# Kernel tuning notes

Measured on AMD Instinct MI355X. Metric: run time of the kernel, lower is better.

The kernel has to match this reference:

```python
import jax, jax.numpy as jnp
import numpy as np
import math

DIM = 512
HEADS = 16
HD = DIM // HEADS
HT, WT = 32, 32          # trained input_resolution
LT = HT * WT             # trained_len
TBL = (2 * HT - 1) * (2 * WT - 1)  # 3969 rows in relative_coords_table
CPB_HID = 512


def _l2norm(a, eps=1e-12):
    n = jnp.linalg.norm(a, axis=-1, keepdims=True)
    return a / jnp.maximum(n, eps)


def setup_inputs() -> dict:
    key = jax.random.key(0)
    ks = jax.random.split(key, 10)
    B, N = 8, 1024
    std = 0.02
    return {
        "x": jax.random.normal(ks[0], (B, N, DIM), jnp.float32),
        "qkv_w": jax.random.normal(ks[1], (3 * DIM, DIM), jnp.float32) * std,
        "qkv_b": jnp.zeros((3 * DIM,), jnp.float32),
        "proj_w": jax.random.normal(ks[2], (DIM, DIM), jnp.float32) * std,
        "proj_b": jnp.zeros((DIM,), jnp.float32),
        # softplus-inverse init: softplus(temperature) == 1/0.24
        "temperature": jnp.log(jnp.exp(jnp.ones((HEADS, 1, 1), jnp.float32) / 0.24) - 1.0),
        "query_embedding": jax.random.normal(ks[3], (HEADS, 1, HD), jnp.float32) * 0.02,
        "cpb_fc1_w": jax.random.normal(ks[4], (CPB_HID, 2), jnp.float32) * std,
        "cpb_fc1_b": jnp.zeros((CPB_HID,), jnp.float32),
        "cpb_fc2_w": jax.random.normal(ks[5], (HEADS, CPB_HID), jnp.float32) * std,
        "cpb_fc2_b": jnp.zeros((HEADS,), jnp.float32),
        "relative_coords_table": jax.random.uniform(ks[6], (TBL, 2), jnp.float32, -1.0, 1.0),
        "relative_pos_index": jax.random.randint(ks[7], (LT * LT,), 0, TBL, jnp.int32),
        "seq_length_scale": jnp.float32(math.log(float(N))),
        "padding_mask": jnp.zeros((B, N), bool),
        "H": 32,
        "W": 32,
    }


def reference(x, qkv_w, qkv_b, proj_w, proj_b, temperature, query_embedding,
              cpb_fc1_w, cpb_fc1_b, cpb_fc2_w, cpb_fc2_b,
              relative_coords_table, seq_length_scale,
              relative_pos_index, padding_mask, H, W):
    B, N, C = x.shape
    # qkv projection -> [B, N, 3, heads, hd] -> per-tensor [B, heads, N, hd]
    qkv = (x @ qkv_w.T + qkv_b).reshape(B, N, 3, HEADS, HD)
    q, k, v = (jnp.transpose(qkv[:, :, i], (0, 2, 1, 3)) for i in range(3))

    # continuous position bias MLP: [TBL, 2] -> [TBL, heads]
    t = jnp.maximum(relative_coords_table @ cpb_fc1_w.T + cpb_fc1_b, 0.0)
    t = t @ cpb_fc2_w.T + cpb_fc2_b                       # [TBL, heads]
    rb = t.T[:, relative_pos_index]                       # [heads, LT*LT]
    rb = rb.reshape(HEADS, LT, HT, WT)
    rb = jax.image.resize(rb, (HEADS, LT, H, W), 'bilinear')   # interp key axis
    rb = rb.reshape(HEADS, LT, N).transpose(0, 2, 1).reshape(HEADS, N, HT, WT)
    rb = jax.image.resize(rb, (HEADS, N, H, W), 'bilinear')    # interp query axis
    rb = rb.reshape(HEADS, N, N).transpose(0, 2, 1)             # [heads, N, N]

    scale = jax.nn.softplus(temperature) * seq_length_scale     # [heads, 1, 1]
    qn = (_l2norm(q) + query_embedding[None]) * scale[None]     # [B, heads, N, hd]
    kn = _l2norm(k)
    attn = jnp.einsum('bhnd,bhmd->bhnm', qn, kn) + rb[None]     # [B, heads, N, N]
    attn = jax.nn.softmax(attn, axis=-1)
    out = jnp.einsum('bhnm,bhmd->bhnd', attn, v)
    out = out.transpose(0, 2, 1, 3).reshape(B, N, C)
    return out @ proj_w.T + proj_b
```

## Files before the change

### kernel.cpp

```cpp
#include <hip/hip_runtime.h>
#include <math.h>

#define BATCH 8
#define NSEQ  1024
#define DIMC  512
#define HEADS 16
#define HD    32
#define TBLN  3969
#define QROWS (BATCH*HEADS*NSEQ)

typedef __attribute__((ext_vector_type(8))) short bf16x8;
typedef __attribute__((ext_vector_type(4))) float f32x4;

__device__ __forceinline__ unsigned short f2bf(float f) {
  union { float f; unsigned u; } c; c.f = f;
  unsigned x = c.u + 0x7fffu + ((c.u >> 16) & 1u);
  return (unsigned short)(x >> 16);
}
__device__ __forceinline__ float bf2f(unsigned short h) {
  union { unsigned u; float f; } c; c.u = ((unsigned)h) << 16; return c.f;
}

__global__ __launch_bounds__(256) void split_kernel(
    const float* __restrict__ src, unsigned short* __restrict__ hi,
    unsigned short* __restrict__ lo, int n4)
{
  int gid = blockIdx.x * 256 + threadIdx.x;
  if (gid >= n4) return;
  float4 v = ((const float4*)src)[gid];
  float vv[4] = {v.x, v.y, v.z, v.w};
  unsigned short h[4], l[4];
#pragma unroll
  for (int i = 0; i < 4; ++i) {
    h[i] = f2bf(vv[i]);
    l[i] = f2bf(vv[i] - bf2f(h[i]));
  }
  uint2 hp, lp;
  hp.x = h[0] | ((unsigned)h[1] << 16); hp.y = h[2] | ((unsigned)h[3] << 16);
  lp.x = l[0] | ((unsigned)l[1] << 16); lp.y = l[2] | ((unsigned)l[3] << 16);
  ((uint2*)hi)[gid] = hp;
  ((uint2*)lo)[gid] = lp;
}

template<int EPI>
__global__ __launch_bounds__(256) void gemm_split_kernel(
    const unsigned short* __restrict__ Ah, const unsigned short* __restrict__ Al,
    const unsigned short* __restrict__ Wh, const unsigned short* __restrict__ Wl,
    const float* __restrict__ bias,
    float* __restrict__ o0p, float* __restrict__ o1p, float* __restrict__ o2p)
{
  const int K = DIMC;
  __shared__ __align__(16) unsigned short lds[4 * 4096];
  unsigned short* ldsAh = lds;
  unsigned short* ldsAl = lds + 4096;
  unsigned short* ldsBh = lds + 8192;
  unsigned short* ldsBl = lds + 12288;
  const int tid = threadIdx.x;
  const int wave = tid >> 6, lane = tid & 63;
  const int l16 = lane & 15, hi4 = lane >> 4;
  const int rowBase = blockIdx.y * 128, colBase = blockIdx.x * 128;
  const int warpRow = (wave >> 1) * 64, warpCol = (wave & 1) * 64;

  const int o0 = wave * 2048 + lane * 16;
  const int o1 = o0 + 1024;
  const int row0 = o0 >> 6, s0 = (o0 >> 4) & 3;
  const int row1 = o1 >> 6, s1 = (o1 >> 4) & 3;
  const int g0 = row0 * K + ((s0 ^ ((row0 >> 1) & 3)) << 3);
  const int g1 = row1 * K + ((s1 ^ ((row1 >> 1) & 3)) << 3);

  const unsigned short* A0h = Ah + (size_t)rowBase * K;
  const unsigned short* A0l = Al + (size_t)rowBase * K;
  const unsigned short* W0h = Wh + (size_t)colBase * K;
  const unsigned short* W0l = Wl + (size_t)colBase * K;

  f32x4 acc[4][4] = {};

  float biasv[4];
#pragma unroll
  for (int fj = 0; fj < 4; ++fj)
    biasv[fj] = bias[colBase + warpCol + fj * 16 + l16];

  int ra[4], rbq[4];
#pragma unroll
  for (int f = 0; f < 4; ++f) {
    int rowA = warpRow + f * 16 + l16;
    ra[f] = rowA * 64 + ((hi4 ^ ((rowA >> 1) & 3)) << 4);
    int rowB = warpCol + f * 16 + l16;
    rbq[f] = rowB * 64 + ((hi4 ^ ((rowB >> 1) & 3)) << 4);
  }

#define GLD(gsrc, ldst) __builtin_amdgcn_global_load_lds( \
      (const __attribute__((address_space(1))) unsigned int*)(gsrc), \
      (__attribute__((address_space(3))) unsigned int*)(ldst), 16, 0, 0)

  for (int k0 = 0; k0 < K; k0 += 32) {
    __syncthreads();
    GLD(A0h + k0 + g0, (char*)ldsAh + o0);
    GLD(A0h + k0 + g1, (char*)ldsAh + o1);
    GLD(A0l + k0 + g0, (char*)ldsAl + o0);
    GLD(A0l + k0 + g1, (char*)ldsAl + o1);
    GLD(W0h + k0 + g0, (char*)ldsBh + o0);
    GLD(W0h + k0 + g1, (char*)ldsBh + o1);
    GLD(W0l + k0 + g0, (char*)ldsBl + o0);
    GLD(W0l + k0 + g1, (char*)ldsBl + o1);
    __syncthreads();

    bf16x8 a_h[4], a_l[4], b_h[4], b_l[4];
#pragma unroll
    for (int f = 0; f < 4; ++f) {
      a_h[f] = *(const bf16x8*)((const char*)ldsAh + ra[f]);
      a_l[f] = *(const bf16x8*)((const char*)ldsAl + ra[f]);
      b_h[f] = *(const bf16x8*)((const char*)ldsBh + rbq[f]);
      b_l[f] = *(const bf16x8*)((const char*)ldsBl + rbq[f]);
    }
#pragma unroll
    for (int fi = 0; fi < 4; ++fi)
#pragma unroll
      for (int fj = 0; fj < 4; ++fj) {
        acc[fi][fj] = __builtin_amdgcn_mfma_f32_16x16x32_bf16(a_l[fi], b_h[fj], acc[fi][fj], 0, 0, 0);
        acc[fi][fj] = __builtin_amdgcn_mfma_f32_16x16x32_bf16(a_h[fi], b_l[fj], acc[fi][fj], 0, 0, 0);
        acc[fi][fj] = __builtin_amdgcn_mfma_f32_16x16x32_bf16(a_h[fi], b_h[fj], acc[fi][fj], 0, 0, 0);
      }
  }
#undef GLD

#pragma unroll
  for (int fi = 0; fi < 4; ++fi)
#pragma unroll
    for (int fj = 0; fj < 4; ++fj)
#pragma unroll
      for (int r = 0; r < 4; ++r) {
        int m = rowBase + warpRow + fi * 16 + hi4 * 4 + r;
        int c = colBase + warpCol + fj * 16 + l16;
        float val = acc[fi][fj][r] + biasv[fj];
        if (EPI == 0) {
          int b = m >> 10, n = m & 1023;
          int which = c >> 9, rem = c & 511;
          int hh = rem >> 5, d = rem & 31;
          float* dst = (which == 0) ? o0p : (which == 1) ? o1p : o2p;
          dst[(((size_t)b * HEADS + hh) * NSEQ + n) * HD + d] = val;
        } else {
          o0p[(size_t)m * DIMC + c] = val;
        }
      }
}

__global__ __launch_bounds__(256) void cpb_kernel(
    const float* __restrict__ table, const float* __restrict__ fc1w,
    const float* __restrict__ fc1b, const float* __restrict__ fc2w,
    const float* __restrict__ fc2b, float* __restrict__ tT)
{
  const int row = blockIdx.x;
  const float c0 = table[row*2], c1 = table[row*2+1];
  __shared__ float hid[512];
  __shared__ float red[256];
  const int tid = threadIdx.x;
  for (int j = tid; j < 512; j += 256)
    hid[j] = fmaxf(fmaf(c0, fc1w[j*2], fmaf(c1, fc1w[j*2+1], fc1b[j])), 0.f);
  __syncthreads();
  const int h = tid & 15, part = tid >> 4;
  float s = 0.f;
#pragma unroll
  for (int jj = 0; jj < 32; ++jj) {
    int j = part*32 + jj;
    s = fmaf(hid[j], fc2w[h*512 + j], s);
  }
  red[tid] = s;
  __syncthreads();
  if (tid < 16) {
    float t = fc2b[tid];
#pragma unroll
    for (int p = 0; p < 16; ++p) t += red[tid + p*16];
    tT[(size_t)tid * TBLN + row] = t;
  }
}

__global__ __launch_bounds__(256) void rb_gather_kernel(
    const float* __restrict__ tT, const int* __restrict__ rpi,
    unsigned short* __restrict__ rb)
{
  int gid = blockIdx.x * 256 + threadIdx.x;
  int idx = rpi[gid];
#pragma unroll
  for (int h = 0; h < 16; ++h)
    rb[(size_t)h * NSEQ * NSEQ + gid] = f2bf(tT[h * TBLN + idx]);
}

__global__ __launch_bounds__(256) void normsplit_kernel(
    const float* __restrict__ qb, const float* __restrict__ kb,
    const float* __restrict__ temperature, const float* __restrict__ qe,
    const float* __restrict__ sls,
    unsigned short* __restrict__ qh, unsigned short* __restrict__ ql,
    unsigned short* __restrict__ kh, unsigned short* __restrict__ kl)
{
  const int gid = blockIdx.x * 256 + threadIdx.x;
  const int lane = gid & 31;
  const int row = gid >> 5;
  const bool isQ = row < QROWS;
  const float* src = isQ ? qb : kb;
  const int r = isQ ? row : row - QROWS;
  float x = src[(size_t)r * HD + lane];
  float ss = x * x;
#pragma unroll
  for (int m = 16; m >= 1; m >>= 1) ss += __shfl_xor(ss, m);
  float y = x / fmaxf(sqrtf(ss), 1e-12f);
  if (isQ) {
    const int h = (r >> 10) & (HEADS - 1);
    float scale = log1pf(__expf(temperature[h])) * sls[0];
    y = (y + qe[h * HD + lane]) * scale;
  }
  unsigned short hi = f2bf(y);
  unsigned short lo = f2bf(y - bf2f(hi));
  size_t idx = (size_t)r * HD + lane;
  if (isQ) { qh[idx] = hi; ql[idx] = lo; }
  else     { kh[idx] = hi; kl[idx] = lo; }
}

__global__ __launch_bounds__(256) void vt_kernel(
    const float* __restrict__ vb, unsigned short* __restrict__ vt)
{
  __shared__ float tile[32][257];
  const int bh = blockIdx.x, ch = blockIdx.y;
  const int t = threadIdx.x;
  const float* src = vb + ((size_t)bh * NSEQ + ch * 256) * HD;
#pragma unroll
  for (int i = 0; i < 32; ++i) {
    int idx = i * 256 + t;
    tile[idx & 31][idx >> 5] = src[idx];
  }
  __syncthreads();
  unsigned short* dst = vt + (size_t)bh * HD * NSEQ + ch * 256;
#pragma unroll
  for (int i = 0; i < 32; ++i) {
    int idx = i * 256 + t;
    int d = idx >> 8, nl = idx & 255;
    dst[(size_t)d * NSEQ + nl] = f2bf(tile[d][nl]);
  }
}

__global__ __launch_bounds__(256, 4) void attn_mfma_kernel(
    const unsigned short* __restrict__ qh, const unsigned short* __restrict__ ql,
    const unsigned short* __restrict__ kh, const unsigned short* __restrict__ kl,
    const unsigned short* __restrict__ vt, const unsigned short* __restrict__ rb,
    unsigned short* __restrict__ aoh, unsigned short* __restrict__ aol)
{
  const int bh = blockIdx.x;
  const int h = bh & (HEADS - 1), b = bh >> 4;
  const int wave = threadIdx.x >> 6;
  const int lane = threadIdx.x & 63;
  const int l16 = lane & 15, hi4 = lane >> 4;
  const int qbase = blockIdx.y * 128 + wave * 32;

  bf16x8 qhf[2], qlf[2];
#pragma unroll
  for (int g = 0; g < 2; ++g) {
    size_t ro = ((size_t)bh * NSEQ + qbase + g * 16 + l16) * HD + hi4 * 8;
    qhf[g] = *(const bf16x8*)(qh + ro);
    qlf[g] = *(const bf16x8*)(ql + ro);
  }

  f32x4 accV[2][2] = {};
  float mst[2] = {-INFINITY, -INFINITY};
  float lst[2] = {0.f, 0.f};

  const int krow_p = 8 * (l16 >> 2) + (l16 & 3);

  for (int kt = 0; kt < NSEQ / 32; ++kt) {
    const int k0 = kt * 32;
    size_t kr0 = ((size_t)bh * NSEQ + k0 + krow_p) * HD + hi4 * 8;
    size_t kr1 = kr0 + 4 * HD;
    bf16x8 kh0 = *(const bf16x8*)(kh + kr0);
    bf16x8 kh1 = *(const bf16x8*)(kh + kr1);
    bf16x8 kl0 = *(const bf16x8*)(kl + kr0);
    bf16x8 kl1 = *(const bf16x8*)(kl + kr1);
    bf16x8 vt0 = *(const bf16x8*)(vt + ((size_t)bh * HD +  0 + l16) * NSEQ + k0 + hi4 * 8);
    bf16x8 vt1 = *(const bf16x8*)(vt + ((size_t)bh * HD + 16 + l16) * NSEQ + k0 + hi4 * 8);

#pragma unroll
    for (int g = 0; g < 2; ++g) {
      f32x4 D0 = {0.f, 0.f, 0.f, 0.f};
      f32x4 D1 = {0.f, 0.f, 0.f, 0.f};
      D0 = __builtin_amdgcn_mfma_f32_16x16x32_bf16(kh0, qhf[g], D0, 0, 0, 0);
      D0 = __builtin_amdgcn_mfma_f32_16x16x32_bf16(kh0, qlf[g], D0, 0, 0, 0);
      D0 = __builtin_amdgcn_mfma_f32_16x16x32_bf16(kl0, qhf[g], D0, 0, 0, 0);
      D1 = __builtin_amdgcn_mfma_f32_16x16x32_bf16(kh1, qhf[g], D1, 0, 0, 0);
      D1 = __builtin_amdgcn_mfma_f32_16x16x32_bf16(kh1, qlf[g], D1, 0, 0, 0);
      D1 = __builtin_amdgcn_mfma_f32_16x16x32_bf16(kl1, qhf[g], D1, 0, 0, 0);

      bf16x8 b8 = *(const bf16x8*)(rb + ((size_t)h * NSEQ + qbase + g * 16 + l16) * NSEQ + k0 + hi4 * 8);

      float sv0[4], sv1[4];
#pragma unroll
      for (int r = 0; r < 4; ++r) {
        sv0[r] = D0[r] + bf2f((unsigned short)b8[r]);
        sv1[r] = D1[r] + bf2f((unsigned short)b8[4 + r]);
      }
      float tm = fmaxf(fmaxf(fmaxf(sv0[0], sv0[1]), fmaxf(sv0[2], sv0[3])),
                       fmaxf(fmaxf(sv1[0], sv1[1]), fmaxf(sv1[2], sv1[3])));
      tm = fmaxf(tm, __shfl_xor(tm, 16));
      tm = fmaxf(tm, __shfl_xor(tm, 32));
      float mn = fmaxf(mst[g], tm);
      float corr = __expf(mst[g] - mn);
      mst[g] = mn;
      float p0[4], p1[4], ps = 0.f;
#pragma unroll
      for (int r = 0; r < 4; ++r) {
        p0[r] = __expf(sv0[r] - mn);
        p1[r] = __expf(sv1[r] - mn);
        ps += p0[r] + p1[r];
      }
      ps += __shfl_xor(ps, 16);
      ps += __shfl_xor(ps, 32);
      lst[g] = lst[g] * corr + ps;

      float cA[4];
#pragma unroll
      for (int r = 0; r < 4; ++r) cA[r] = __shfl(corr, hi4 * 4 + r);
#pragma unroll
      for (int r = 0; r < 4; ++r) {
        accV[g][0][r] *= cA[r];
        accV[g][1][r] *= cA[r];
      }
      bf16x8 pa;
#pragma unroll
      for (int r = 0; r < 4; ++r) {
        pa[r]     = (short)f2bf(p0[r]);
        pa[4 + r] = (short)f2bf(p1[r]);
      }
      accV[g][0] = __builtin_amdgcn_mfma_f32_16x16x32_bf16(pa, vt0, accV[g][0], 0, 0, 0);
      accV[g][1] = __builtin_amdgcn_mfma_f32_16x16x32_bf16(pa, vt1, accV[g][1], 0, 0, 0);
    }
  }

#pragma unroll
  for (int g = 0; g < 2; ++g) {
    float inv = 1.f / lst[g];
    float iA[4];
#pragma unroll
    for (int r = 0; r < 4; ++r) iA[r] = __shfl(inv, hi4 * 4 + r);
#pragma unroll
    for (int df = 0; df < 2; ++df)
#pragma unroll
      for (int r = 0; r < 4; ++r) {
        size_t idx = ((size_t)b * NSEQ + qbase + g * 16 + hi4 * 4 + r) * DIMC
                     + h * HD + df * 16 + l16;
        float val = accV[g][df][r] * iA[r];
        unsigned short hh = f2bf(val);
        aoh[idx] = hh;
        aol[idx] = f2bf(val - bf2f(hh));
      }
  }
}

extern "C" void kernel_launch(void* const* d_in, const int* in_sizes, int n_in,
                              void* d_out, int out_size, void* d_ws, size_t ws_size,
                              hipStream_t stream)
{
  (void)in_sizes; (void)n_in; (void)out_size; (void)ws_size;
  const float* x      = (const float*)d_in[0];
  const float* qkv_w  = (const float*)d_in[1];
  const float* qkv_b  = (const float*)d_in[2];
  const float* proj_w = (const float*)d_in[3];
  const float* proj_b = (const float*)d_in[4];
  const float* temp   = (const float*)d_in[5];
  const float* qe     = (const float*)d_in[6];
  const float* fc1w   = (const float*)d_in[7];
  const float* fc1b   = (const float*)d_in[8];
  const float* fc2w   = (const float*)d_in[9];
  const float* fc2b   = (const float*)d_in[10];
  const float* tbl    = (const float*)d_in[11];
  const int*   rpi    = (const int*)d_in[12];
  const float* sls    = (const float*)d_in[13];

  char* ws = (char*)d_ws;
  const size_t perT = (size_t)BATCH * HEADS * NSEQ * HD;
  float* qb = (float*)ws;
  float* kb = qb + perT;
  float* vb = kb + perT;
  float* tT = vb + perT;
  unsigned short* qh = (unsigned short*)(tT + 65536);
  unsigned short* ql = qh + perT;
  unsigned short* kh = ql + perT;
  unsigned short* kl = kh + perT;
  unsigned short* vt = kl + perT;
  unsigned short* xh = vt + perT;
  unsigned short* xl = xh + perT;
  unsigned short* pwh = xl + perT;
  unsigned short* pwl = pwh + 262144;
  unsigned short* qwh = qh;
  unsigned short* qwl = qh + 786432;
  unsigned short* rb  = (unsigned short*)qb;
  unsigned short* aoh = xh;
  unsigned short* aol = xl;

  split_kernel<<<dim3(4096), 256, 0, stream>>>(x, xh, xl, 1048576);
  split_kernel<<<dim3(768),  256, 0, stream>>>(qkv_w, qwh, qwl, 196608);
  split_kernel<<<dim3(256),  256, 0, stream>>>(proj_w, pwh, pwl, 65536);
  gemm_split_kernel<0><<<dim3(12, 64), 256, 0, stream>>>(
      xh, xl, qwh, qwl, qkv_b, qb, kb, vb);
  cpb_kernel<<<dim3(TBLN), 256, 0, stream>>>(tbl, fc1w, fc1b, fc2w, fc2b, tT);
  normsplit_kernel<<<dim3((2*QROWS*32)/256), 256, 0, stream>>>(
      qb, kb, temp, qe, sls, qh, ql, kh, kl);
  vt_kernel<<<dim3(BATCH*HEADS, NSEQ/256), 256, 0, stream>>>(vb, vt);
  rb_gather_kernel<<<dim3((NSEQ*NSEQ)/256), 256, 0, stream>>>(tT, rpi, rb);
  attn_mfma_kernel<<<dim3(BATCH*HEADS, NSEQ/128), 256, 0, stream>>>(
      qh, ql, kh, kl, vt, rb, aoh, aol);
  gemm_split_kernel<1><<<dim3(4, 64), 256, 0, stream>>>(
      aoh, aol, pwh, pwl, proj_b, (float*)d_out, nullptr, nullptr);
}
```

Baseline: 380.2 us.

## Replace online softmax with static per-row max bound and MFMA row sums

Drops the running-max online softmax in the attention kernel. A fixed upper bound per query row is computed ahead of time from the query norm (keys are unit-norm) plus the row max of the bias, so the loop no longer needs max reductions, rescale factors or accumulator corrections. Row sums now come from an extra MFMA against a ones vector, exponentials use exp2 with log2e folded into the bias, and bf16 packing uses v_cvt_pk_bf16_f32. This adds a small rowmax kernel and a qmag output. If the bound is loose, the exponentials can underflow and lose precision.

```diff
diff --git a/kernel.cpp b/kernel.cpp
--- a/kernel.cpp
+++ b/kernel.cpp
@@ -8,6 +8,7 @@
 #define HD    32
 #define TBLN  3969
 #define QROWS (BATCH*HEADS*NSEQ)
+#define LOG2E 1.4426950408889634f
 
 typedef __attribute__((ext_vector_type(8))) short bf16x8;
 typedef __attribute__((ext_vector_type(4))) float f32x4;
@@ -19,6 +20,11 @@
 }
 __device__ __forceinline__ float bf2f(unsigned short h) {
   union { unsigned u; float f; } c; c.u = ((unsigned)h) << 16; return c.f;
+}
+__device__ __forceinline__ unsigned cvt_pk_bf16(float lo, float hi) {
+  unsigned r;
+  asm("v_cvt_pk_bf16_f32 %0, %1, %2" : "=v"(r) : "v"(lo), "v"(hi));
+  return r;
 }
 
 __global__ __launch_bounds__(256) void split_kernel(
@@ -183,7 +189,26 @@
   int idx = rpi[gid];
 #pragma unroll
   for (int h = 0; h < 16; ++h)
-    rb[(size_t)h * NSEQ * NSEQ + gid] = f2bf(tT[h * TBLN + idx]);
+    rb[(size_t)h * NSEQ * NSEQ + gid] = f2bf(tT[h * TBLN + idx] * LOG2E);
+}
+
+__global__ __launch_bounds__(256) void rowmax_kernel(
+    const unsigned short* __restrict__ rb, float* __restrict__ rbmax)
+{
+  const int row = blockIdx.x * 4 + (threadIdx.x >> 6);
+  const int lane = threadIdx.x & 63;
+  const unsigned short* src = rb + (size_t)row * NSEQ + lane * 16;
+  bf16x8 a = *(const bf16x8*)src;
+  bf16x8 b = *(const bf16x8*)(src + 8);
+  float m = -1e30f;
+#pragma unroll
+  for (int j = 0; j < 8; ++j) {
+    m = fmaxf(m, bf2f((unsigned short)a[j]));
+    m = fmaxf(m, bf2f((unsigned short)b[j]));
+  }
+#pragma unroll
+  for (int s = 32; s >= 1; s >>= 1) m = fmaxf(m, __shfl_xor(m, s));
+  if (lane == 0) rbmax[row] = m;
 }
 
 __global__ __launch_bounds__(256) void normsplit_kernel(
@@ -191,7 +216,8 @@
     const float* __restrict__ temperature, const float* __restrict__ qe,
     const float* __restrict__ sls,
     unsigned short* __restrict__ qh, unsigned short* __restrict__ ql,
-    unsigned short* __restrict__ kh, unsigned short* __restrict__ kl)
+    unsigned short* __restrict__ kh, unsigned short* __restrict__ kl,
+    float* __restrict__ qmag)
 {
   const int gid = blockIdx.x * 256 + threadIdx.x;
   const int lane = gid & 31;
@@ -208,6 +234,10 @@
     const int h = (r >> 10) & (HEADS - 1);
     float scale = log1pf(__expf(temperature[h])) * sls[0];
     y = (y + qe[h * HD + lane]) * scale;
+    float s2 = y * y;
+#pragma unroll
+    for (int m = 16; m >= 1; m >>= 1) s2 += __shfl_xor(s2, m);
+    if (lane == 0) qmag[r] = sqrtf(s2);
   }
   unsigned short hi = f2bf(y);
   unsigned short lo = f2bf(y - bf2f(hi));
@@ -242,6 +272,7 @@
     const unsigned short* __restrict__ qh, const unsigned short* __restrict__ ql,
     const unsigned short* __restrict__ kh, const unsigned short* __restrict__ kl,
     const unsigned short* __restrict__ vt, const unsigned short* __restrict__ rb,
+    const float* __restrict__ qmag, const float* __restrict__ rbmax,
     unsigned short* __restrict__ aoh, unsigned short* __restrict__ aol)
 {
   const int bh = blockIdx.x;
@@ -252,16 +283,23 @@
   const int qbase = blockIdx.y * 128 + wave * 32;
 
   bf16x8 qhf[2], qlf[2];
+  float Ms[2];
 #pragma unroll
   for (int g = 0; g < 2; ++g) {
-    size_t ro = ((size_t)bh * NSEQ + qbase + g * 16 + l16) * HD + hi4 * 8;
+    const int qrow = qbase + g * 16 + l16;
+    size_t ro = ((size_t)bh * NSEQ + qrow) * HD + hi4 * 8;
     qhf[g] = *(const bf16x8*)(qh + ro);
     qlf[g] = *(const bf16x8*)(ql + ro);
-  }
+    Ms[g] = qmag[(size_t)bh * NSEQ + qrow] * (1.01f * LOG2E)
+            + rbmax[h * NSEQ + qrow] + 0.2f;
+  }
+
+  bf16x8 ones;
+#pragma unroll
+  for (int j = 0; j < 8; ++j) ones[j] = (short)0x3f80;
 
   f32x4 accV[2][2] = {};
-  float mst[2] = {-INFINITY, -INFINITY};
-  float lst[2] = {0.f, 0.f};
+  f32x4 accL[2] = {};
 
   const int krow_p = 8 * (l16 >> 2) + (l16 & 3);
 
@@ -289,67 +327,41 @@
 
       bf16x8 b8 = *(const bf16x8*)(rb + ((size_t)h * NSEQ + qbase + g * 16 + l16) * NSEQ + k0 + hi4 * 8);
 
-      float sv0[4], sv1[4];
+      float p0[4], p1[4];
 #pragma unroll
       for (int r = 0; r < 4; ++r) {
-        sv0[r] = D0[r] + bf2f((unsigned short)b8[r]);
-        sv1[r] = D1[r] + bf2f((unsigned short)b8[4 + r]);
+        float a0 = fmaf(D0[r], LOG2E, bf2f((unsigned short)b8[r]))     - Ms[g];
+        float a1 = fmaf(D1[r], LOG2E, bf2f((unsigned short)b8[4 + r])) - Ms[g];
+        p0[r] = __builtin_amdgcn_exp2f(a0);
+        p1[r] = __builtin_amdgcn_exp2f(a1);
       }
-      float tm = fmaxf(fmaxf(fmaxf(sv0[0], sv0[1]), fmaxf(sv0[2], sv0[3])),
-                       fmaxf(fmaxf(sv1[0], sv1[1]), fmaxf(sv1[2], sv1[3])));
-      tm = fmaxf(tm, __shfl_xor(tm, 16));
-      tm = fmaxf(tm, __shfl_xor(tm, 32));
-      float mn = fmaxf(mst[g], tm);
-      float corr = __expf(mst[g] - mn);
-      mst[g] = mn;
-      float p0[4], p1[4], ps = 0.f;
-#pragma unroll
-      for (int r = 0; r < 4; ++r) {
-        p0[r] = __expf(sv0[r] - mn);
-        p1[r] = __expf(sv1[r] - mn);
-        ps += p0[r] + p1[r];
-      }
-      ps += __shfl_xor(ps, 16);
-      ps += __shfl_xor(ps, 32);
-      lst[g] = lst[g] * corr + ps;
-
-      float cA[4];
-#pragma unroll
-      for (int r = 0; r < 4; ++r) cA[r] = __shfl(corr, hi4 * 4 + r);
-#pragma unroll
-      for (int r = 0; r < 4; ++r) {
-        accV[g][0][r] *= cA[r];
-        accV[g][1][r] *= cA[r];
-      }
-      bf16x8 pa;
-#pragma unroll
-      for (int r = 0; r < 4; ++r) {
-        pa[r]     = (short)f2bf(p0[r]);
-        pa[4 + r] = (short)f2bf(p1[r]);
-      }
-      accV[g][0] = __builtin_amdgcn_mfma_f32_16x16x32_bf16(pa, vt0, accV[g][0], 0, 0, 0);
-      accV[g][1] = __builtin_amdgcn_mfma_f32_16x16x32_bf16(pa, vt1, accV[g][1], 0, 0, 0);
+      union { bf16x8 v; unsigned u[4]; } pa;
+      pa.u[0] = cvt_pk_bf16(p0[0], p0[1]);
+      pa.u[1] = cvt_pk_bf16(p0[2], p0[3]);
+      pa.u[2] = cvt_pk_bf16(p1[0], p1[1]);
+      pa.u[3] = cvt_pk_bf16(p1[2], p1[3]);
+
+      accV[g][0] = __builtin_amdgcn_mfma_f32_16x16x32_bf16(pa.v, vt0, accV[g][0], 0, 0, 0);
+      accV[g][1] = __builtin_amdgcn_mfma_f32_16x16x32_bf16(pa.v, vt1, accV[g][1], 0, 0, 0);
+      accL[g]    = __builtin_amdgcn_mfma_f32_16x16x32_bf16(pa.v, ones, accL[g], 0, 0, 0);
     }
   }
 
 #pragma unroll
-  for (int g = 0; g < 2; ++g) {
-    float inv = 1.f / lst[g];
-    float iA[4];
-#pragma unroll
-    for (int r = 0; r < 4; ++r) iA[r] = __shfl(inv, hi4 * 4 + r);
-#pragma unroll
-    for (int df = 0; df < 2; ++df)
-#pragma unroll
-      for (int r = 0; r < 4; ++r) {
+  for (int g = 0; g < 2; ++g)
+#pragma unroll
+    for (int r = 0; r < 4; ++r) {
+      float inv = 1.f / accL[g][r];
+#pragma unroll
+      for (int df = 0; df < 2; ++df) {
         size_t idx = ((size_t)b * NSEQ + qbase + g * 16 + hi4 * 4 + r) * DIMC
                      + h * HD + df * 16 + l16;
-        float val = accV[g][df][r] * iA[r];
+        float val = accV[g][df][r] * inv;
         unsigned short hh = f2bf(val);
         aoh[idx] = hh;
         aol[idx] = f2bf(val - bf2f(hh));
       }
-  }
+    }
 }
 
 extern "C" void kernel_launch(void* const* d_in, const int* in_sizes, int n_in,
@@ -387,6 +399,8 @@
   unsigned short* xl = xh + perT;
   unsigned short* pwh = xl + perT;
   unsigned short* pwl = pwh + 262144;
+  float* rbmax = (float*)(pwl + 262144);
+  float* qmag  = rbmax + 16384;
   unsigned short* qwh = qh;
   unsigned short* qwl = qh + 786432;
   unsigned short* rb  = (unsigned short*)qb;
@@ -400,11 +414,12 @@
       xh, xl, qwh, qwl, qkv_b, qb, kb, vb);
   cpb_kernel<<<dim3(TBLN), 256, 0, stream>>>(tbl, fc1w, fc1b, fc2w, fc2b, tT);
   normsplit_kernel<<<dim3((2*QROWS*32)/256), 256, 0, stream>>>(
-      qb, kb, temp, qe, sls, qh, ql, kh, kl);
+      qb, kb, temp, qe, sls, qh, ql, kh, kl, qmag);
   vt_kernel<<<dim3(BATCH*HEADS, NSEQ/256), 256, 0, stream>>>(vb, vt);
   rb_gather_kernel<<<dim3((NSEQ*NSEQ)/256), 256, 0, stream>>>(tT, rpi, rb);
+  rowmax_kernel<<<dim3(HEADS*NSEQ/4), 256, 0, stream>>>(rb, rbmax);
   attn_mfma_kernel<<<dim3(BATCH*HEADS, NSEQ/128), 256, 0, stream>>>(
-      qh, ql, kh, kl, vt, rb, aoh, aol);
+      qh, ql, kh, kl, vt, rb, qmag, rbmax, aoh, aol);
   gemm_split_kernel<1><<<dim3(4, 64), 256, 0, stream>>>(
       aoh, aol, pwh, pwl, proj_b, (float*)d_out, nullptr, nullptr);
 }
```

After: 384.0 us. No clear change (+1.0%).
